# Optimization experiments

Hardware: AMD Instinct MI355X
Metric: run time of the kernel (lower is better)

## Reference

```python
import jax, jax.numpy as jnp
import numpy as np
import math

N = 50000       # nodes
E = 800000      # edges
C_IN = 64
C_OUT = 32
N_SH = 9        # (l_max+1)^2 with l_max=2
H = 32          # radial_hidden_dim


def spherical_harmonics(vectors):
    # vectors: [..., 3] -> [..., 9]; faithful to source incl. (x+iy).real == x
    norm = jnp.clip(jnp.linalg.norm(vectors, axis=-1, keepdims=True), 1e-8)
    d = vectors / norm
    x, y, z = d[..., 0], d[..., 1], d[..., 2]
    c00 = 0.5 / math.sqrt(math.pi)
    c1 = 0.5 * math.sqrt(3.0 / (2.0 * math.pi))
    c1z = 0.5 * math.sqrt(3.0 / math.pi)
    c2 = 0.25 * math.sqrt(15.0 / (2.0 * math.pi))
    c2z = 0.5 * math.sqrt(15.0 / (2.0 * math.pi))
    c20 = 0.25 * math.sqrt(5.0 / math.pi)
    feats = [
        c00 * jnp.ones_like(x),
        -c1 * x,                      # -0.5*sqrt(3/2pi)*(x+iy).real
        c1z * z,
        c1 * x,                       # 0.5*sqrt(3/2pi)*(x-iy).real
        c2 * (x * x - y * y),         # 0.25*sqrt(15/2pi)*((x+iy)^2).real
        -c2z * z * x,
        c20 * (2.0 * z * z - x * x - y * y),
        c2z * z * x,
        c2 * (x * x - y * y),
    ]
    return jnp.stack(feats, axis=-1)


def setup_inputs() -> dict:
    key = jax.random.key(0)
    ks = jax.random.split(key, 9)
    features = jax.random.normal(ks[0], (N, C_IN), dtype=jnp.float32)
    positions = jax.random.normal(ks[1], (N, 3), dtype=jnp.float32)
    edge_index = jax.random.randint(ks[2], (2, E), 0, N, dtype=jnp.int64)
    fan1 = N_SH + C_IN  # 73 (intended fan-in of first radial layer)
    W1 = jax.random.normal(ks[3], (fan1, H), dtype=jnp.float32) / math.sqrt(fan1)
    b1 = jnp.zeros((H,), dtype=jnp.float32)
    W2 = jax.random.normal(ks[4], (H, H), dtype=jnp.float32) / math.sqrt(H)
    b2 = jnp.zeros((H,), dtype=jnp.float32)
    W3 = jax.random.normal(ks[5], (H, N_SH * C_OUT), dtype=jnp.float32) / math.sqrt(H)
    b3 = jnp.zeros((N_SH * C_OUT,), dtype=jnp.float32)
    return {"features": features, "positions": positions, "W1": W1, "b1": b1,
            "W2": W2, "b2": b2, "W3": W3, "b3": b3, "edge_index": edge_index}


def reference(features, positions, W1, b1, W2, b2, W3, b3, edge_index):
    row, col = edge_index[0], edge_index[1]
    rel_pos = positions[row] - positions[col]                 # [E,3]
    dist = jnp.clip(jnp.linalg.norm(rel_pos, axis=-1, keepdims=True), 1e-8)
    directions = rel_pos / dist
    y_ij = spherical_harmonics(directions)                    # [E,9]
    combined = jnp.concatenate([y_ij, features[col]], axis=-1)  # [E,9+C_IN]
    h = jax.nn.silu(combined @ W1 + b1)
    h = jax.nn.silu(h @ W2 + b2)
    messages = h @ W3 + b3                                    # [E,9*C_OUT]
    msg = messages.reshape(-1, N_SH, C_OUT).sum(axis=1)       # [E,C_OUT]
    out = jax.ops.segment_sum(msg, row, num_segments=features.shape[0])
    return out
```

## Files before the change

### kernel.cpp

```cpp
#include <hip/hip_runtime.h>
#include <hip/hip_fp16.h>

#define NNODES 50000
#define NEDGES 800000
#define CIN 64
#define COUT 32
#define NSH 9
#define HDIM 32

#define NT_BLOCKS 6250
#define HIST_BLOCKS 782
#define SCAN_BLOCKS 125
#define SCAN_CHUNK 400

typedef _Float16 half2v __attribute__((ext_vector_type(2)));

__device__ __forceinline__ unsigned pkrtz(float a, float b) {
    return __builtin_bit_cast(unsigned, __builtin_amdgcn_cvt_pkrtz(a, b));
}
__device__ __forceinline__ float dot2f(unsigned a, unsigned b, float c) {
    return __builtin_amdgcn_fdot2(__builtin_bit_cast(half2v, a),
                                  __builtin_bit_cast(half2v, b), c, false);
}

__device__ __forceinline__ void prep_body(
    int t, const float* __restrict__ W3, const float* __restrict__ b3,
    const float* __restrict__ W1, const float* __restrict__ b1,
    const float* __restrict__ W2,
    float* __restrict__ W3s, float* __restrict__ b3s, float* __restrict__ prm,
    unsigned* __restrict__ w2p, unsigned* __restrict__ w3sp)
{
    if (t < HDIM * COUT) {
        int k = t >> 5, c = t & 31;
        float s = 0.f;
        #pragma unroll
        for (int q = 0; q < NSH; ++q) s += W3[k * (NSH * COUT) + q * COUT + c];
        W3s[t] = s;
    }
    if (t < 512) {
        int kk = t >> 5, c = t & 31;
        w2p[t] = pkrtz(W2[(2 * kk) * HDIM + c], W2[(2 * kk + 1) * HDIM + c]);
        float s0 = 0.f, s1 = 0.f;
        #pragma unroll
        for (int q = 0; q < NSH; ++q) {
            s0 += W3[(2 * kk) * (NSH * COUT) + q * COUT + c];
            s1 += W3[(2 * kk + 1) * (NSH * COUT) + q * COUT + c];
        }
        w3sp[t] = pkrtz(s0, s1);
    }
    if (t < COUT) {
        float s = 0.f;
        #pragma unroll
        for (int q = 0; q < NSH; ++q) s += b3[q * COUT + t];
        b3s[t] = s;
    }
    if (t < HDIM) {
        const float c00 = 0.28209479177387814f;
        const float c1  = 0.3454941494713355f;
        const float c1z = 0.4886025119029199f;
        const float c2  = 0.38627420202318958f;
        const float c2z = 0.7725484040463791f;
        const float c20 = 0.31539156525252005f;
        prm[t]       = b1[t] + c00 * W1[0 * HDIM + t];
        prm[32 + t]  = c1  * (W1[3 * HDIM + t] - W1[1 * HDIM + t]);
        prm[64 + t]  = c1z *  W1[2 * HDIM + t];
        prm[96 + t]  = c2z * (W1[7 * HDIM + t] - W1[5 * HDIM + t]);
        prm[128 + t] = c2  * (W1[4 * HDIM + t] + W1[8 * HDIM + t]);
        prm[160 + t] = c20 *  W1[6 * HDIM + t];
    }
}

__global__ void prep_w3(const float* __restrict__ W3, const float* __restrict__ b3,
                        const float* __restrict__ W1, const float* __restrict__ b1,
                        const float* __restrict__ W2,
                        float* __restrict__ W3s, float* __restrict__ b3s,
                        float* __restrict__ prm,
                        unsigned* __restrict__ w2p, unsigned* __restrict__ w3sp) {
    prep_body(threadIdx.x, W3, b3, W1, b1, W2, W3s, b3s, prm, w2p, w3sp);
}

__global__ __launch_bounds__(256) void nt_hist(
    const float* __restrict__ feat, const float* __restrict__ W1,
    const int* __restrict__ ei, __half* __restrict__ g1h,
    int* __restrict__ cnt, int do_nt)
{
    int b = blockIdx.x;
    if (do_nt && b < NT_BLOCKS) {
        int tid = b * 256 + threadIdx.x;
        int n = tid >> 5, c = tid & 31;
        if (n < NNODES) {
            float acc = 0.f;
            const float* fr = feat + (size_t)n * CIN;
            const float* wp = W1 + NSH * HDIM + c;
            #pragma unroll 8
            for (int k = 0; k < CIN; ++k)
                acc = fmaf(fr[k], wp[k * HDIM], acc);
            g1h[(size_t)n * HDIM + c] = __float2half(acc);
        }
    } else {
        int hb = do_nt ? (b - NT_BLOCKS) : b;
        int e4 = (hb * 256 + threadIdx.x) * 4;
        if (e4 < NEDGES) {
            int4 r = *reinterpret_cast<const int4*>(ei + e4);
            atomicAdd(&cnt[r.x], 1);
            atomicAdd(&cnt[r.y], 1);
            atomicAdd(&cnt[r.z], 1);
            atomicAdd(&cnt[r.w], 1);
        }
    }
}

__global__ __launch_bounds__(256) void scan_bsum(const int* __restrict__ cnt,
                                                 int* __restrict__ bsum) {
    int b = blockIdx.x, t = threadIdx.x;
    int base = b * SCAN_CHUNK;
    int s = 0;
    for (int i = t; i < SCAN_CHUNK; i += 256) s += cnt[base + i];
    #pragma unroll
    for (int d = 32; d > 0; d >>= 1) s += __shfl_down(s, d);
    __shared__ int l4[4];
    if ((t & 63) == 0) l4[t >> 6] = s;
    __syncthreads();
    if (t == 0) bsum[b] = l4[0] + l4[1] + l4[2] + l4[3];
}

__global__ __launch_bounds__(1024) void scan_top_prep(
    const int* __restrict__ bsum, int* __restrict__ ebsum, int* __restrict__ off,
    const float* __restrict__ W3, const float* __restrict__ b3,
    const float* __restrict__ W1, const float* __restrict__ b1,
    const float* __restrict__ W2,
    float* __restrict__ W3s, float* __restrict__ b3s, float* __restrict__ prm,
    unsigned* __restrict__ w2p, unsigned* __restrict__ w3sp)
{
    if (blockIdx.x == 1) {
        prep_body(threadIdx.x, W3, b3, W1, b1, W2, W3s, b3s, prm, w2p, w3sp);
        return;
    }
    __shared__ int lds[128];
    int t = threadIdx.x;
    if (t < 128) lds[t] = (t < SCAN_BLOCKS) ? bsum[t] : 0;
    __syncthreads();
    for (int d = 1; d < 128; d <<= 1) {
        int u = (t >= d && t < 128) ? lds[t - d] : 0;
        __syncthreads();
        if (t < 128) lds[t] += u;
        __syncthreads();
    }
    if (t < SCAN_BLOCKS) ebsum[t] = (t == 0) ? 0 : lds[t - 1];
    if (t == 0) off[NNODES] = NEDGES;
}

__global__ __launch_bounds__(256) void scan_offsets(const int* __restrict__ cnt,
                                                    const int* __restrict__ ebsum,
                                                    int* __restrict__ off,
                                                    int* __restrict__ cursor) {
    int b = blockIdx.x, t = threadIdx.x;
    int base = b * SCAN_CHUNK;
    __shared__ int lds[256];
    int2 c2 = make_int2(0, 0);
    if (t < SCAN_CHUNK / 2) c2 = reinterpret_cast<const int2*>(cnt + base)[t];
    int ps = c2.x + c2.y;
    lds[t] = ps;
    __syncthreads();
    for (int d = 1; d < 256; d <<= 1) {
        int u = (t >= d) ? lds[t - d] : 0;
        __syncthreads();
        lds[t] += u;
        __syncthreads();
    }
    int excl = lds[t] - ps;
    if (t < SCAN_CHUNK / 2) {
        int o = ebsum[b] + excl;
        int2 w = make_int2(o, o + c2.x);
        reinterpret_cast<int2*>(off + base)[t] = w;
        reinterpret_cast<int2*>(cursor + base)[t] = w;
    }
}

__device__ __forceinline__ float fast_silu(float v) {
    return v * __builtin_amdgcn_rcpf(1.f + __expf(-v));
}

__global__ __launch_bounds__(256) void edge_compute_g1(
    const __half* __restrict__ g1h, const float* __restrict__ pos,
    const float* __restrict__ prm,
    const unsigned* __restrict__ w2p, const float* __restrict__ b2,
    const unsigned* __restrict__ w3sp, const float* __restrict__ b3s,
    const int* __restrict__ ei, int* __restrict__ cursor,
    unsigned int* __restrict__ msg)
{
    int e = blockIdx.x * blockDim.x + threadIdx.x;
    if (e >= NEDGES) return;
    int row = ei[e];
    int col = ei[NEDGES + e];

    int slot = atomicAdd(&cursor[row], 1);
    unsigned int* mp = msg + (size_t)slot * 16;

    float px = pos[3 * row + 0] - pos[3 * col + 0];
    float py = pos[3 * row + 1] - pos[3 * col + 1];
    float pz = pos[3 * row + 2] - pos[3 * col + 2];
    float r2 = px * px + py * py + pz * pz;
    float rs = (r2 >= 1e-16f) ? __builtin_amdgcn_rsqf(r2) : 0.f;
    float x = px * rs, y = py * rs, z = pz * rs;

    float zx = z * x;
    float xxyy = x * x - y * y;
    float w6 = 2.f * z * z - x * x - y * y;

    const float* b1e = prm;
    const float* A = prm + 32;
    const float* B = prm + 64;
    const float* C = prm + 96;
    const float* D = prm + 128;
    const float* E = prm + 160;

    float h1[HDIM];
    const uint4* g4 = reinterpret_cast<const uint4*>(g1h + (size_t)col * HDIM);
    #pragma unroll
    for (int q = 0; q < 4; ++q) {
        uint4 u = g4[q];
        const unsigned int uw[4] = {u.x, u.y, u.z, u.w};
        #pragma unroll
        for (int j = 0; j < 4; ++j) {
            float2 f = __half22float2(*reinterpret_cast<const __half2*>(&uw[j]));
            h1[8 * q + 2 * j]     = f.x;
            h1[8 * q + 2 * j + 1] = f.y;
        }
    }
    #pragma unroll
    for (int c = 0; c < HDIM; ++c) {
        float v = h1[c] + b1e[c];
        v = fmaf(x, A[c], v);
        v = fmaf(z, B[c], v);
        v = fmaf(zx, C[c], v);
        v = fmaf(xxyy, D[c], v);
        v = fmaf(w6, E[c], v);
        h1[c] = fast_silu(v);
    }
    unsigned h1p[HDIM / 2];
    #pragma unroll
    for (int q = 0; q < HDIM / 2; ++q) h1p[q] = pkrtz(h1[2 * q], h1[2 * q + 1]);

    float h2[HDIM];
    #pragma unroll
    for (int c = 0; c < HDIM; ++c) h2[c] = b2[c];
    #pragma unroll
    for (int kk = 0; kk < HDIM / 2; ++kk) {
        unsigned hp = h1p[kk];
        #pragma unroll
        for (int c = 0; c < HDIM; ++c)
            h2[c] = dot2f(hp, w2p[kk * HDIM + c], h2[c]);
    }
    unsigned h2p[HDIM / 2];
    #pragma unroll
    for (int q = 0; q < HDIM / 2; ++q)
        h2p[q] = pkrtz(fast_silu(h2[2 * q]), fast_silu(h2[2 * q + 1]));

    float m[COUT];
    #pragma unroll
    for (int c = 0; c < COUT; ++c) m[c] = b3s[c];
    #pragma unroll
    for (int kk = 0; kk < HDIM / 2; ++kk) {
        unsigned hp = h2p[kk];
        #pragma unroll
        for (int c = 0; c < COUT; ++c)
            m[c] = dot2f(hp, w3sp[kk * COUT + c], m[c]);
    }

    uint4 pk[4];
    unsigned int* pu = reinterpret_cast<unsigned int*>(pk);
    #pragma unroll
    for (int q = 0; q < 16; ++q) pu[q] = pkrtz(m[2 * q], m[2 * q + 1]);
    uint4* mp4 = reinterpret_cast<uint4*>(mp);
    #pragma unroll
    for (int q = 0; q < 4; ++q) mp4[q] = pk[q];
}

__global__ __launch_bounds__(256) void gather_kernel(
    const unsigned int* __restrict__ msg, const int* __restrict__ off,
    float* __restrict__ out)
{
    int node = blockIdx.x * 4 + (threadIdx.x >> 6);
    if (node >= NNODES) return;
    int lane = threadIdx.x & 63;
    int g = lane >> 4, p = lane & 15;
    int s0 = off[node], s1 = off[node + 1];
    float ax = 0.f, ay = 0.f;
    for (int s = s0 + g; s < s1; s += 4) {
        unsigned int u = msg[(size_t)s * 16 + p];
        __half2 h = *reinterpret_cast<__half2*>(&u);
        ax += __low2float(h);
        ay += __high2float(h);
    }
    ax += __shfl_xor(ax, 16); ay += __shfl_xor(ay, 16);
    ax += __shfl_xor(ax, 32); ay += __shfl_xor(ay, 32);
    if (lane < 16)
        reinterpret_cast<float2*>(out + (size_t)node * COUT)[p] = make_float2(ax, ay);
}

__global__ __launch_bounds__(256) void edge_atomic_kernel(
    const float* __restrict__ feat, const float* __restrict__ pos,
    const float* __restrict__ W1, const float* __restrict__ b1,
    const float* __restrict__ W2, const float* __restrict__ b2,
    const float* __restrict__ W3s, const float* __restrict__ b3s,
    const int* __restrict__ ei, float* __restrict__ out)
{
    int e = blockIdx.x * blockDim.x + threadIdx.x;
    if (e >= NEDGES) return;
    int row = ei[e];
    int col = ei[NEDGES + e];

    float px = pos[3 * row + 0] - pos[3 * col + 0];
    float py = pos[3 * row + 1] - pos[3 * col + 1];
    float pz = pos[3 * row + 2] - pos[3 * col + 2];
    float r2 = px * px + py * py + pz * pz;
    float rs = (r2 >= 1e-16f) ? __builtin_amdgcn_rsqf(r2) : 0.f;
    float x = px * rs, y = py * rs, z = pz * rs;

    const float c00 = 0.28209479177387814f;
    const float c1  = 0.3454941494713355f;
    const float c1z = 0.4886025119029199f;
    const float c2  = 0.38627420202318958f;
    const float c2z = 0.7725484040463791f;
    const float c20 = 0.31539156525252005f;

    float sh[NSH];
    float xxyy = x * x - y * y;
    float zx = z * x;
    sh[0] = c00;
    sh[1] = -c1 * x;
    sh[2] = c1z * z;
    sh[3] = c1 * x;
    sh[4] = c2 * xxyy;
    sh[5] = -c2z * zx;
    sh[6] = c20 * (2.f * z * z - x * x - y * y);
    sh[7] = c2z * zx;
    sh[8] = c2 * xxyy;

    float h1[HDIM];
    #pragma unroll
    for (int c = 0; c < HDIM; ++c) h1[c] = b1[c];
    #pragma unroll
    for (int k = 0; k < NSH; ++k) {
        float v = sh[k];
        #pragma unroll
        for (int c = 0; c < HDIM; ++c) h1[c] = fmaf(v, W1[k * HDIM + c], h1[c]);
    }
    const float4* f4 = reinterpret_cast<const float4*>(feat + (size_t)col * CIN);
    for (int kk = 0; kk < CIN / 4; ++kk) {
        float4 f = f4[kk];
        const float* Wp = W1 + (NSH + kk * 4) * HDIM;
        #pragma unroll
        for (int c = 0; c < HDIM; ++c) h1[c] = fmaf(f.x, Wp[c], h1[c]);
        #pragma unroll
        for (int c = 0; c < HDIM; ++c) h1[c] = fmaf(f.y, Wp[HDIM + c], h1[c]);
        #pragma unroll
        for (int c = 0; c < HDIM; ++c) h1[c] = fmaf(f.z, Wp[2 * HDIM + c], h1[c]);
        #pragma unroll
        for (int c = 0; c < HDIM; ++c) h1[c] = fmaf(f.w, Wp[3 * HDIM + c], h1[c]);
    }
    #pragma unroll
    for (int c = 0; c < HDIM; ++c) h1[c] = fast_silu(h1[c]);

    float h2[HDIM];
    #pragma unroll
    for (int c = 0; c < HDIM; ++c) h2[c] = b2[c];
    for (int k = 0; k < HDIM; ++k) {
        float v = h1[k];
        #pragma unroll
        for (int c = 0; c < HDIM; ++c) h2[c] = fmaf(v, W2[k * HDIM + c], h2[c]);
    }
    #pragma unroll
    for (int c = 0; c < HDIM; ++c) h2[c] = fast_silu(h2[c]);

    float m[COUT];
    #pragma unroll
    for (int c = 0; c < COUT; ++c) m[c] = b3s[c];
    for (int k = 0; k < HDIM; ++k) {
        float v = h2[k];
        #pragma unroll
        for (int c = 0; c < COUT; ++c) m[c] = fmaf(v, W3s[k * COUT + c], m[c]);
    }

    float* op = out + (size_t)row * COUT;
    #pragma unroll
    for (int c = 0; c < COUT; ++c) atomicAdd(op + c, m[c]);
}

extern "C" void kernel_launch(void* const* d_in, const int* in_sizes, int n_in,
                              void* d_out, int out_size, void* d_ws, size_t ws_size,
                              hipStream_t stream) {
    const float* feat = (const float*)d_in[0];
    const float* pos  = (const float*)d_in[1];
    const float* W1   = (const float*)d_in[2];
    const float* b1   = (const float*)d_in[3];
    const float* W2   = (const float*)d_in[4];
    const float* b2   = (const float*)d_in[5];
    const float* W3   = (const float*)d_in[6];
    const float* b3   = (const float*)d_in[7];
    const int*   ei   = (const int*)d_in[8];
    float* outf = (float*)d_out;

    int* cnt    = (int*)d_ws;
    int* off    = cnt + NNODES;
    int* cursor = off + NNODES + 2;
    int* bsum   = cursor + NNODES;
    int* ebsum  = bsum + 128;
    const size_t head_ints = ((size_t)NNODES + (NNODES + 2) + NNODES + 128 + 128 + 3) & ~(size_t)3;
    float* fbase = (float*)(((int*)d_ws) + head_ints);
    float* W3s = fbase;
    float* b3s = W3s + HDIM * COUT;
    float* prm = b3s + COUT;
    unsigned* w2p  = (unsigned*)(prm + 192);
    unsigned* w3sp = w2p + 512;
    const size_t head_floats = HDIM * COUT + COUT + 192 + 1024;
    __half* g1h = (__half*)(fbase + head_floats);
    unsigned int* msg = (unsigned int*)(g1h + (size_t)NNODES * HDIM);
    size_t need = (head_ints + head_floats) * 4
                + (size_t)NNODES * HDIM * 2
                + (size_t)NEDGES * 64;

    if (ws_size >= need) {
        (void)hipMemsetAsync(cnt, 0, (size_t)NNODES * sizeof(int), stream);
        nt_hist<<<NT_BLOCKS + HIST_BLOCKS, 256, 0, stream>>>(feat, W1, ei, g1h, cnt, 1);
        scan_bsum<<<SCAN_BLOCKS, 256, 0, stream>>>(cnt, bsum);
        scan_top_prep<<<2, 1024, 0, stream>>>(bsum, ebsum, off, W3, b3, W1, b1, W2,
                                              W3s, b3s, prm, w2p, w3sp);
        scan_offsets<<<SCAN_BLOCKS, 256, 0, stream>>>(cnt, ebsum, off, cursor);
        edge_compute_g1<<<(NEDGES + 255) / 256, 256, 0, stream>>>(
            g1h, pos, prm, w2p, b2, w3sp, b3s, ei, cursor, msg);
        gather_kernel<<<(NNODES + 3) / 4, 256, 0, stream>>>(msg, off, outf);
    } else {
        (void)hipMemsetAsync(d_out, 0, (size_t)out_size * sizeof(float), stream);
        prep_w3<<<1, 1024, 0, stream>>>(W3, b3, W1, b1, W2, W3s, b3s, prm, w2p, w3sp);
        edge_atomic_kernel<<<(NEDGES + 255) / 256, 256, 0, stream>>>(
            feat, pos, W1, b1, W2, b2, W3s, b3s, ei, outf);
    }
}
```

Baseline: 156.9 us.

## Coalesce edge-kernel gathers and scatters via LDS staging and padded positions

The edge kernel now cooperatively loads each edge's 64-byte g1 row through lane shuffles, so four lanes fetch one row's four 16-byte chunks into shared memory. The packed output messages are staged in LDS and written back the same cooperative way, replacing one thread writing 64 scattered bytes. Positions are repacked into float4 by extra blocks in the first kernel, so each node's position is a single vector load. The changes aim at uncoalesced per-thread gather/scatter traffic, at the cost of 40KB of LDS per block (which may cut occupancy), an extra repack pass, and removal of the bounds check, which depends on E being a multiple of 256.

```diff
diff --git a/kernel.cpp b/kernel.cpp
--- a/kernel.cpp
+++ b/kernel.cpp
@@ -9,6 +9,7 @@
 #define HDIM 32
 
 #define NT_BLOCKS 6250
+#define P4_BLOCKS 196
 #define HIST_BLOCKS 782
 #define SCAN_BLOCKS 125
 #define SCAN_CHUNK 400
@@ -81,6 +82,7 @@
 
 __global__ __launch_bounds__(256) void nt_hist(
     const float* __restrict__ feat, const float* __restrict__ W1,
+    const float* __restrict__ pos, float4* __restrict__ pos4,
     const int* __restrict__ ei, __half* __restrict__ g1h,
     int* __restrict__ cnt, int do_nt)
 {
@@ -97,8 +99,12 @@
                 acc = fmaf(fr[k], wp[k * HDIM], acc);
             g1h[(size_t)n * HDIM + c] = __float2half(acc);
         }
+    } else if (do_nt && b < NT_BLOCKS + P4_BLOCKS) {
+        int n = (b - NT_BLOCKS) * 256 + threadIdx.x;
+        if (n < NNODES)
+            pos4[n] = make_float4(pos[3 * n], pos[3 * n + 1], pos[3 * n + 2], 0.f);
     } else {
-        int hb = do_nt ? (b - NT_BLOCKS) : b;
+        int hb = do_nt ? (b - NT_BLOCKS - P4_BLOCKS) : b;
         int e4 = (hb * 256 + threadIdx.x) * 4;
         if (e4 < NEDGES) {
             int4 r = *reinterpret_cast<const int4*>(ei + e4);
@@ -182,24 +188,34 @@
 }
 
 __global__ __launch_bounds__(256) void edge_compute_g1(
-    const __half* __restrict__ g1h, const float* __restrict__ pos,
+    const __half* __restrict__ g1h, const float4* __restrict__ pos4,
     const float* __restrict__ prm,
     const unsigned* __restrict__ w2p, const float* __restrict__ b2,
     const unsigned* __restrict__ w3sp, const float* __restrict__ b3s,
     const int* __restrict__ ei, int* __restrict__ cursor,
     unsigned int* __restrict__ msg)
 {
-    int e = blockIdx.x * blockDim.x + threadIdx.x;
-    if (e >= NEDGES) return;
+    __shared__ uint4 lsg[4][64][5];
+    __shared__ uint4 lsm[4][64][5];
+    int tid = threadIdx.x;
+    int w = tid >> 6, l = tid & 63;
+    int e = blockIdx.x * 256 + tid;
     int row = ei[e];
     int col = ei[NEDGES + e];
 
     int slot = atomicAdd(&cursor[row], 1);
-    unsigned int* mp = msg + (size_t)slot * 16;
-
-    float px = pos[3 * row + 0] - pos[3 * col + 0];
-    float py = pos[3 * row + 1] - pos[3 * col + 1];
-    float pz = pos[3 * row + 2] - pos[3 * col + 2];
+
+    int p = l & 3, qh = l >> 2;
+    #pragma unroll
+    for (int k = 0; k < 4; ++k) {
+        int src = 16 * k + qh;
+        int colq = __shfl(col, src);
+        uint4 v = reinterpret_cast<const uint4*>(g1h + (size_t)colq * HDIM)[p];
+        lsg[w][src][p] = v;
+    }
+
+    float4 pr = pos4[row], pc = pos4[col];
+    float px = pr.x - pc.x, py = pr.y - pc.y, pz = pr.z - pc.z;
     float r2 = px * px + py * py + pz * pz;
     float rs = (r2 >= 1e-16f) ? __builtin_amdgcn_rsqf(r2) : 0.f;
     float x = px * rs, y = py * rs, z = pz * rs;
@@ -216,16 +232,15 @@
     const float* E = prm + 160;
 
     float h1[HDIM];
-    const uint4* g4 = reinterpret_cast<const uint4*>(g1h + (size_t)col * HDIM);
-    #pragma unroll
-    for (int q = 0; q < 4; ++q) {
-        uint4 u = g4[q];
+    #pragma unroll
+    for (int j = 0; j < 4; ++j) {
+        uint4 u = lsg[w][l][j];
         const unsigned int uw[4] = {u.x, u.y, u.z, u.w};
         #pragma unroll
-        for (int j = 0; j < 4; ++j) {
-            float2 f = __half22float2(*reinterpret_cast<const __half2*>(&uw[j]));
-            h1[8 * q + 2 * j]     = f.x;
-            h1[8 * q + 2 * j + 1] = f.y;
+        for (int i = 0; i < 4; ++i) {
+            float2 f = __half22float2(*reinterpret_cast<const __half2*>(&uw[i]));
+            h1[8 * j + 2 * i]     = f.x;
+            h1[8 * j + 2 * i + 1] = f.y;
         }
     }
     #pragma unroll
@@ -268,13 +283,22 @@
             m[c] = dot2f(hp, w3sp[kk * COUT + c], m[c]);
     }
 
-    uint4 pk[4];
-    unsigned int* pu = reinterpret_cast<unsigned int*>(pk);
-    #pragma unroll
-    for (int q = 0; q < 16; ++q) pu[q] = pkrtz(m[2 * q], m[2 * q + 1]);
-    uint4* mp4 = reinterpret_cast<uint4*>(mp);
-    #pragma unroll
-    for (int q = 0; q < 4; ++q) mp4[q] = pk[q];
+    #pragma unroll
+    for (int j = 0; j < 4; ++j) {
+        uint4 v;
+        v.x = pkrtz(m[8 * j + 0], m[8 * j + 1]);
+        v.y = pkrtz(m[8 * j + 2], m[8 * j + 3]);
+        v.z = pkrtz(m[8 * j + 4], m[8 * j + 5]);
+        v.w = pkrtz(m[8 * j + 6], m[8 * j + 7]);
+        lsm[w][l][j] = v;
+    }
+    #pragma unroll
+    for (int k = 0; k < 4; ++k) {
+        int src = 16 * k + qh;
+        int slotq = __shfl(slot, src);
+        uint4 v = lsm[w][src][p];
+        reinterpret_cast<uint4*>(msg + (size_t)slotq * 16)[p] = v;
+    }
 }
 
 __global__ __launch_bounds__(256) void gather_kernel(
@@ -415,21 +439,24 @@
     unsigned* w2p  = (unsigned*)(prm + 192);
     unsigned* w3sp = w2p + 512;
     const size_t head_floats = HDIM * COUT + COUT + 192 + 1024;
-    __half* g1h = (__half*)(fbase + head_floats);
+    float4* pos4 = (float4*)(fbase + head_floats);
+    __half* g1h = (__half*)(pos4 + NNODES);
     unsigned int* msg = (unsigned int*)(g1h + (size_t)NNODES * HDIM);
     size_t need = (head_ints + head_floats) * 4
+                + (size_t)NNODES * 16
                 + (size_t)NNODES * HDIM * 2
                 + (size_t)NEDGES * 64;
 
     if (ws_size >= need) {
         (void)hipMemsetAsync(cnt, 0, (size_t)NNODES * sizeof(int), stream);
-        nt_hist<<<NT_BLOCKS + HIST_BLOCKS, 256, 0, stream>>>(feat, W1, ei, g1h, cnt, 1);
+        nt_hist<<<NT_BLOCKS + P4_BLOCKS + HIST_BLOCKS, 256, 0, stream>>>(
+            feat, W1, pos, pos4, ei, g1h, cnt, 1);
         scan_bsum<<<SCAN_BLOCKS, 256, 0, stream>>>(cnt, bsum);
         scan_top_prep<<<2, 1024, 0, stream>>>(bsum, ebsum, off, W3, b3, W1, b1, W2,
                                               W3s, b3s, prm, w2p, w3sp);
         scan_offsets<<<SCAN_BLOCKS, 256, 0, stream>>>(cnt, ebsum, off, cursor);
-        edge_compute_g1<<<(NEDGES + 255) / 256, 256, 0, stream>>>(
-            g1h, pos, prm, w2p, b2, w3sp, b3s, ei, cursor, msg);
+        edge_compute_g1<<<NEDGES / 256, 256, 0, stream>>>(
+            g1h, pos4, prm, w2p, b2, w3sp, b3s, ei, cursor, msg);
         gather_kernel<<<(NNODES + 3) / 4, 256, 0, stream>>>(msg, off, outf);
     } else {
         (void)hipMemsetAsync(d_out, 0, (size_t)out_size * sizeof(float), stream);
```

Result: slower. 161.5 us (+3.0%).

## Bin edges by destination node range before edge MLP and pad positions to float4

Applied to the files above, without the earlier changes.

Adds a bin_scatter pass that groups edges into 8 bins by destination-node range, so the edge MLP kernel processes edges whose rows fall in a narrow node range. This is meant to make message writes and cursor atomics more local, which helps cache and DRAM locality. Positions are also padded to float4 so each position is one vector load. The cost is an extra kernel, an 8-byte-per-edge intermediate buffer, and more workspace. A fallback path is kept for when workspace is smaller.

```diff
diff --git a/kernel.cpp b/kernel.cpp
--- a/kernel.cpp
+++ b/kernel.cpp
@@ -9,9 +9,14 @@
 #define HDIM 32
 
 #define NT_BLOCKS 6250
+#define P4_BLOCKS 196
 #define HIST_BLOCKS 782
 #define SCAN_BLOCKS 125
 #define SCAN_CHUNK 400
+#define NBINS 8
+#define NODES_PER_BIN 6250
+#define BIN_BLOCKS 3125
+#define EDGE_BPB 412
 
 typedef _Float16 half2v __attribute__((ext_vector_type(2)));
 
@@ -81,6 +86,7 @@
 
 __global__ __launch_bounds__(256) void nt_hist(
     const float* __restrict__ feat, const float* __restrict__ W1,
+    const float* __restrict__ pos, float4* __restrict__ pos4,
     const int* __restrict__ ei, __half* __restrict__ g1h,
     int* __restrict__ cnt, int do_nt)
 {
@@ -97,8 +103,12 @@
                 acc = fmaf(fr[k], wp[k * HDIM], acc);
             g1h[(size_t)n * HDIM + c] = __float2half(acc);
         }
+    } else if (do_nt && b < NT_BLOCKS + P4_BLOCKS) {
+        int n = (b - NT_BLOCKS) * 256 + threadIdx.x;
+        if (n < NNODES)
+            pos4[n] = make_float4(pos[3 * n], pos[3 * n + 1], pos[3 * n + 2], 0.f);
     } else {
-        int hb = do_nt ? (b - NT_BLOCKS) : b;
+        int hb = do_nt ? (b - NT_BLOCKS - P4_BLOCKS) : b;
         int e4 = (hb * 256 + threadIdx.x) * 4;
         if (e4 < NEDGES) {
             int4 r = *reinterpret_cast<const int4*>(ei + e4);
@@ -153,7 +163,8 @@
 __global__ __launch_bounds__(256) void scan_offsets(const int* __restrict__ cnt,
                                                     const int* __restrict__ ebsum,
                                                     int* __restrict__ off,
-                                                    int* __restrict__ cursor) {
+                                                    int* __restrict__ cursor,
+                                                    int* __restrict__ binCursor) {
     int b = blockIdx.x, t = threadIdx.x;
     int base = b * SCAN_CHUNK;
     __shared__ int lds[256];
@@ -174,32 +185,43 @@
         int2 w = make_int2(o, o + c2.x);
         reinterpret_cast<int2*>(off + base)[t] = w;
         reinterpret_cast<int2*>(cursor + base)[t] = w;
-    }
+        int node = base + 2 * t;
+        if (node % NODES_PER_BIN == 0) binCursor[node / NODES_PER_BIN] = o;
+    }
+}
+
+__global__ __launch_bounds__(256) void bin_scatter(const int* __restrict__ ei,
+                                                   int* __restrict__ binCursor,
+                                                   int2* __restrict__ binbuf) {
+    __shared__ int cnt8[NBINS], base8[NBINS];
+    int t = threadIdx.x;
+    if (t < NBINS) cnt8[t] = 0;
+    __syncthreads();
+    int e = blockIdx.x * 256 + t;
+    int row = ei[e];
+    int col = ei[NEDGES + e];
+    int bin = row / NODES_PER_BIN;
+    int lo = atomicAdd(&cnt8[bin], 1);
+    __syncthreads();
+    if (t < NBINS) base8[t] = atomicAdd(&binCursor[t], cnt8[t]);
+    __syncthreads();
+    binbuf[base8[bin] + lo] = make_int2(row, col);
 }
 
 __device__ __forceinline__ float fast_silu(float v) {
     return v * __builtin_amdgcn_rcpf(1.f + __expf(-v));
 }
 
-__global__ __launch_bounds__(256) void edge_compute_g1(
-    const __half* __restrict__ g1h, const float* __restrict__ pos,
+__device__ __forceinline__ void mlp_body(
+    int row, int col,
+    const __half* __restrict__ g1h, const float4* __restrict__ pos4,
     const float* __restrict__ prm,
     const unsigned* __restrict__ w2p, const float* __restrict__ b2,
     const unsigned* __restrict__ w3sp, const float* __restrict__ b3s,
-    const int* __restrict__ ei, int* __restrict__ cursor,
-    unsigned int* __restrict__ msg)
-{
-    int e = blockIdx.x * blockDim.x + threadIdx.x;
-    if (e >= NEDGES) return;
-    int row = ei[e];
-    int col = ei[NEDGES + e];
-
-    int slot = atomicAdd(&cursor[row], 1);
-    unsigned int* mp = msg + (size_t)slot * 16;
-
-    float px = pos[3 * row + 0] - pos[3 * col + 0];
-    float py = pos[3 * row + 1] - pos[3 * col + 1];
-    float pz = pos[3 * row + 2] - pos[3 * col + 2];
+    uint4* pk)
+{
+    float4 pr = pos4[row], pc = pos4[col];
+    float px = pr.x - pc.x, py = pr.y - pc.y, pz = pr.z - pc.z;
     float r2 = px * px + py * py + pz * pz;
     float rs = (r2 >= 1e-16f) ? __builtin_amdgcn_rsqf(r2) : 0.f;
     float x = px * rs, y = py * rs, z = pz * rs;
@@ -268,11 +290,60 @@
             m[c] = dot2f(hp, w3sp[kk * COUT + c], m[c]);
     }
 
+    #pragma unroll
+    for (int j = 0; j < 4; ++j) {
+        pk[j].x = pkrtz(m[8 * j + 0], m[8 * j + 1]);
+        pk[j].y = pkrtz(m[8 * j + 2], m[8 * j + 3]);
+        pk[j].z = pkrtz(m[8 * j + 4], m[8 * j + 5]);
+        pk[j].w = pkrtz(m[8 * j + 6], m[8 * j + 7]);
+    }
+}
+
+__global__ __launch_bounds__(256) void edge_compute_binned(
+    const __half* __restrict__ g1h, const float4* __restrict__ pos4,
+    const float* __restrict__ prm,
+    const unsigned* __restrict__ w2p, const float* __restrict__ b2,
+    const unsigned* __restrict__ w3sp, const float* __restrict__ b3s,
+    const int2* __restrict__ binbuf, const int* __restrict__ off,
+    int* __restrict__ cursor, unsigned int* __restrict__ msg)
+{
+    int bin = blockIdx.x & (NBINS - 1);
+    int chunk = blockIdx.x >> 3;
+    int binS = off[bin * NODES_PER_BIN];
+    int binE = off[bin * NODES_PER_BIN + NODES_PER_BIN];
+    int i = binS + chunk * 256 + threadIdx.x;
+    if (i >= binE) return;
+
+    int2 rc = binbuf[i];
+    int row = rc.x, col = rc.y;
+    int slot = atomicAdd(&cursor[row], 1);
+
     uint4 pk[4];
-    unsigned int* pu = reinterpret_cast<unsigned int*>(pk);
-    #pragma unroll
-    for (int q = 0; q < 16; ++q) pu[q] = pkrtz(m[2 * q], m[2 * q + 1]);
-    uint4* mp4 = reinterpret_cast<uint4*>(mp);
+    mlp_body(row, col, g1h, pos4, prm, w2p, b2, w3sp, b3s, pk);
+
+    uint4* mp4 = reinterpret_cast<uint4*>(msg + (size_t)slot * 16);
+    #pragma unroll
+    for (int q = 0; q < 4; ++q) mp4[q] = pk[q];
+}
+
+__global__ __launch_bounds__(256) void edge_compute_g1(
+    const __half* __restrict__ g1h, const float4* __restrict__ pos4,
+    const float* __restrict__ prm,
+    const unsigned* __restrict__ w2p, const float* __restrict__ b2,
+    const unsigned* __restrict__ w3sp, const float* __restrict__ b3s,
+    const int* __restrict__ ei, int* __restrict__ cursor,
+    unsigned int* __restrict__ msg)
+{
+    int e = blockIdx.x * blockDim.x + threadIdx.x;
+    if (e >= NEDGES) return;
+    int row = ei[e];
+    int col = ei[NEDGES + e];
+    int slot = atomicAdd(&cursor[row], 1);
+
+    uint4 pk[4];
+    mlp_body(row, col, g1h, pos4, prm, w2p, b2, w3sp, b3s, pk);
+
+    uint4* mp4 = reinterpret_cast<uint4*>(msg + (size_t)slot * 16);
     #pragma unroll
     for (int q = 0; q < 4; ++q) mp4[q] = pk[q];
 }
@@ -402,12 +473,13 @@
     const int*   ei   = (const int*)d_in[8];
     float* outf = (float*)d_out;
 
-    int* cnt    = (int*)d_ws;
-    int* off    = cnt + NNODES;
-    int* cursor = off + NNODES + 2;
-    int* bsum   = cursor + NNODES;
-    int* ebsum  = bsum + 128;
-    const size_t head_ints = ((size_t)NNODES + (NNODES + 2) + NNODES + 128 + 128 + 3) & ~(size_t)3;
+    int* cnt     = (int*)d_ws;
+    int* off     = cnt + NNODES;
+    int* cursor  = off + NNODES + 2;
+    int* bsum    = cursor + NNODES;
+    int* ebsum   = bsum + 128;
+    int* binCur  = ebsum + 128;
+    const size_t head_ints = ((size_t)NNODES + (NNODES + 2) + NNODES + 128 + 128 + 8 + 3) & ~(size_t)3;
     float* fbase = (float*)(((int*)d_ws) + head_ints);
     float* W3s = fbase;
     float* b3s = W3s + HDIM * COUT;
@@ -415,22 +487,40 @@
     unsigned* w2p  = (unsigned*)(prm + 192);
     unsigned* w3sp = w2p + 512;
     const size_t head_floats = HDIM * COUT + COUT + 192 + 1024;
-    __half* g1h = (__half*)(fbase + head_floats);
-    unsigned int* msg = (unsigned int*)(g1h + (size_t)NNODES * HDIM);
-    size_t need = (head_ints + head_floats) * 4
-                + (size_t)NNODES * HDIM * 2
-                + (size_t)NEDGES * 64;
-
-    if (ws_size >= need) {
+    float4* pos4 = (float4*)(fbase + head_floats);
+    __half* g1h  = (__half*)(pos4 + NNODES);
+    int2*  binbuf = (int2*)(g1h + (size_t)NNODES * HDIM);
+    unsigned int* msgA = (unsigned int*)(binbuf + NEDGES);
+    unsigned int* msgB = (unsigned int*)(binbuf);
+    size_t base_need = (head_ints + head_floats) * 4
+                     + (size_t)NNODES * 16
+                     + (size_t)NNODES * HDIM * 2;
+    size_t needA = base_need + (size_t)NEDGES * 8 + (size_t)NEDGES * 64;
+    size_t needB = base_need + (size_t)NEDGES * 64;
+
+    if (ws_size >= needA) {
         (void)hipMemsetAsync(cnt, 0, (size_t)NNODES * sizeof(int), stream);
-        nt_hist<<<NT_BLOCKS + HIST_BLOCKS, 256, 0, stream>>>(feat, W1, ei, g1h, cnt, 1);
+        nt_hist<<<NT_BLOCKS + P4_BLOCKS + HIST_BLOCKS, 256, 0, stream>>>(
+            feat, W1, pos, pos4, ei, g1h, cnt, 1);
         scan_bsum<<<SCAN_BLOCKS, 256, 0, stream>>>(cnt, bsum);
         scan_top_prep<<<2, 1024, 0, stream>>>(bsum, ebsum, off, W3, b3, W1, b1, W2,
                                               W3s, b3s, prm, w2p, w3sp);
-        scan_offsets<<<SCAN_BLOCKS, 256, 0, stream>>>(cnt, ebsum, off, cursor);
+        scan_offsets<<<SCAN_BLOCKS, 256, 0, stream>>>(cnt, ebsum, off, cursor, binCur);
+        bin_scatter<<<BIN_BLOCKS, 256, 0, stream>>>(ei, binCur, binbuf);
+        edge_compute_binned<<<NBINS * EDGE_BPB, 256, 0, stream>>>(
+            g1h, pos4, prm, w2p, b2, w3sp, b3s, binbuf, off, cursor, msgA);
+        gather_kernel<<<(NNODES + 3) / 4, 256, 0, stream>>>(msgA, off, outf);
+    } else if (ws_size >= needB) {
+        (void)hipMemsetAsync(cnt, 0, (size_t)NNODES * sizeof(int), stream);
+        nt_hist<<<NT_BLOCKS + P4_BLOCKS + HIST_BLOCKS, 256, 0, stream>>>(
+            feat, W1, pos, pos4, ei, g1h, cnt, 1);
+        scan_bsum<<<SCAN_BLOCKS, 256, 0, stream>>>(cnt, bsum);
+        scan_top_prep<<<2, 1024, 0, stream>>>(bsum, ebsum, off, W3, b3, W1, b1, W2,
+                                              W3s, b3s, prm, w2p, w3sp);
+        scan_offsets<<<SCAN_BLOCKS, 256, 0, stream>>>(cnt, ebsum, off, cursor, binCur);
         edge_compute_g1<<<(NEDGES + 255) / 256, 256, 0, stream>>>(
-            g1h, pos, prm, w2p, b2, w3sp, b3s, ei, cursor, msg);
-        gather_kernel<<<(NNODES + 3) / 4, 256, 0, stream>>>(msg, off, outf);
+            g1h, pos4, prm, w2p, b2, w3sp, b3s, ei, cursor, msgB);
+        gather_kernel<<<(NNODES + 3) / 4, 256, 0, stream>>>(msgB, off, outf);
     } else {
         (void)hipMemsetAsync(d_out, 0, (size_t)out_size * sizeof(float), stream);
         prep_w3<<<1, 1024, 0, stream>>>(W3, b3, W1, b1, W2, W3s, b3s, prm, w2p, w3sp);
```

Measured after the change: 186.6 us. +19.0%, slower.
